# Kernel optimization log

Measured on AMD Instinct MI355X. Metric: run time of the kernel, lower is better.

## Reference

```python
import jax, jax.numpy as jnp
import numpy as np


def setup_inputs() -> dict:
    key = jax.random.key(0)
    x = jax.random.normal(key, (8192, 4096), dtype=jnp.float32)
    return {"x": x}


def reference(x) -> jnp.ndarray:
    # Sparsemax along the last axis (dim=-1), matching the torch module's math.
    n = x.shape[-1]
    x = x - jnp.max(x, axis=-1, keepdims=True)
    # sort descending
    zs = jnp.flip(jnp.sort(x, axis=-1), axis=-1)  # [B, N]
    r = jnp.arange(1, n + 1, dtype=x.dtype)       # [N]
    bound = 1.0 + r * zs
    cum_zs = jnp.cumsum(zs, axis=-1)
    is_gt = (bound > cum_zs).astype(x.dtype)
    k = jnp.max(is_gt * r, axis=-1, keepdims=True)          # support size
    taus = (jnp.sum(is_gt * zs, axis=-1, keepdims=True) - 1.0) / k
    return jnp.maximum(jnp.zeros_like(x), x - taus)
```

## Files before the change

### kernel.cpp

```cpp
#include <hip/hip_runtime.h>


#define COLS 4096
#define THREADS 256
#define NW 4
#define CAND_CAP 1024
#define MAX_ITERS 32

typedef float f32x4 __attribute__((ext_vector_type(4)));

__global__ __launch_bounds__(THREADS) void sparsemax_kernel(
    const float* __restrict__ x, float* __restrict__ out) {
  __shared__ float cand[CAND_CAP];
  __shared__ float wmax[NW];
  __shared__ float wsum[NW];
  __shared__ int wcnt[NW];
  __shared__ int cnt;

  const int tid = threadIdx.x;
  const int lane = tid & 63;
  const int wid = tid >> 6;
  const long row = blockIdx.x;

  const f32x4* __restrict__ xr =
      reinterpret_cast<const f32x4*>(x + row * COLS);
  f32x4* __restrict__ outr = reinterpret_cast<f32x4*>(out + row * COLS);

  if (tid == 0) cnt = 0;

  f32x4 v0 = xr[tid];
  f32x4 v1 = xr[tid + THREADS];
  f32x4 v2 = xr[tid + 2 * THREADS];
  f32x4 v3 = xr[tid + 3 * THREADS];

  float m = fmaxf(fmaxf(v0.x, v0.y), fmaxf(v0.z, v0.w));
  m = fmaxf(m, fmaxf(fmaxf(v1.x, v1.y), fmaxf(v1.z, v1.w)));
  m = fmaxf(m, fmaxf(fmaxf(v2.x, v2.y), fmaxf(v2.z, v2.w)));
  m = fmaxf(m, fmaxf(fmaxf(v3.x, v3.y), fmaxf(v3.z, v3.w)));
#pragma unroll
  for (int off = 32; off > 0; off >>= 1) m = fmaxf(m, __shfl_xor(m, off));
  if (lane == 0) wmax[wid] = m;
  __syncthreads();
  m = fmaxf(fmaxf(wmax[0], wmax[1]), fmaxf(wmax[2], wmax[3]));

  const float thr = m - 1.0f;

#define EMIT(val)                                   \
  if ((val) > thr) {                                \
    int p = atomicAdd(&cnt, 1);                     \
    if (p < CAND_CAP) cand[p] = (val);              \
  }
  EMIT(v0.x) EMIT(v0.y) EMIT(v0.z) EMIT(v0.w)
  EMIT(v1.x) EMIT(v1.y) EMIT(v1.z) EMIT(v1.w)
  EMIT(v2.x) EMIT(v2.y) EMIT(v2.z) EMIT(v2.w)
  EMIT(v3.x) EMIT(v3.y) EMIT(v3.z) EMIT(v3.w)
#undef EMIT
  __syncthreads();
  const int nc = cnt;

  float tau = thr;
  if (nc <= CAND_CAP) {
    for (int it = 0; it < MAX_ITERS; ++it) {
      float s = 0.0f;
      int c = 0;
      for (int k = lane; k < nc; k += 64) {
        float q = cand[k];
        if (q > tau) { s += q; c += 1; }
      }
#pragma unroll
      for (int off = 32; off > 0; off >>= 1) {
        s += __shfl_xor(s, off);
        c += __shfl_xor(c, off);
      }
      float ntau = (s - 1.0f) / (float)c;
      if (ntau == tau) break;
      tau = ntau;
    }
  } else {
    for (int it = 0; it < MAX_ITERS; ++it) {
      float s = 0.0f;
      int c = 0;
#define ACC(val)                      \
  if ((val) > tau) { s += (val); c += 1; }
      ACC(v0.x) ACC(v0.y) ACC(v0.z) ACC(v0.w)
      ACC(v1.x) ACC(v1.y) ACC(v1.z) ACC(v1.w)
      ACC(v2.x) ACC(v2.y) ACC(v2.z) ACC(v2.w)
      ACC(v3.x) ACC(v3.y) ACC(v3.z) ACC(v3.w)
#undef ACC
#pragma unroll
      for (int off = 32; off > 0; off >>= 1) {
        s += __shfl_xor(s, off);
        c += __shfl_xor(c, off);
      }
      if (lane == 0) { wsum[wid] = s; wcnt[wid] = c; }
      __syncthreads();
      s = wsum[0] + wsum[1] + wsum[2] + wsum[3];
      c = wcnt[0] + wcnt[1] + wcnt[2] + wcnt[3];
      float ntau = (s - 1.0f) / (float)c;
      __syncthreads();
      if (ntau == tau) break;
      tau = ntau;
    }
  }

  f32x4 o;
  o.x = fmaxf(v0.x - tau, 0.0f); o.y = fmaxf(v0.y - tau, 0.0f);
  o.z = fmaxf(v0.z - tau, 0.0f); o.w = fmaxf(v0.w - tau, 0.0f);
  __builtin_nontemporal_store(o, outr + tid);
  o.x = fmaxf(v1.x - tau, 0.0f); o.y = fmaxf(v1.y - tau, 0.0f);
  o.z = fmaxf(v1.z - tau, 0.0f); o.w = fmaxf(v1.w - tau, 0.0f);
  __builtin_nontemporal_store(o, outr + tid + THREADS);
  o.x = fmaxf(v2.x - tau, 0.0f); o.y = fmaxf(v2.y - tau, 0.0f);
  o.z = fmaxf(v2.z - tau, 0.0f); o.w = fmaxf(v2.w - tau, 0.0f);
  __builtin_nontemporal_store(o, outr + tid + 2 * THREADS);
  o.x = fmaxf(v3.x - tau, 0.0f); o.y = fmaxf(v3.y - tau, 0.0f);
  o.z = fmaxf(v3.z - tau, 0.0f); o.w = fmaxf(v3.w - tau, 0.0f);
  __builtin_nontemporal_store(o, outr + tid + 3 * THREADS);
}

extern "C" void kernel_launch(void* const* d_in, const int* in_sizes, int n_in,
                              void* d_out, int out_size, void* d_ws,
                              size_t ws_size, hipStream_t stream) {
  const float* x = (const float*)d_in[0];
  float* out = (float*)d_out;
  const int rows = in_sizes[0] / COLS;
  sparsemax_kernel<<<rows, THREADS, 0, stream>>>(x, out);
}
```

Measured before the change: 231.3 us.

## Split sparsemax into a tau-computation kernel and a separate apply kernel

Splits the fused kernel in two. The first kernel reads each row, finds the threshold tau (only wave 0 iterates over the candidate list) and writes it to workspace. The second kernel rereads x, applies max(x - tau, 0) across four rows per block and writes the output. The intent is to shorten the critical path of each kernel, but it adds a second full read of the input and a kernel launch.

```diff
diff --git a/kernel.cpp b/kernel.cpp
--- a/kernel.cpp
+++ b/kernel.cpp
@@ -6,25 +6,25 @@
 #define NW 4
 #define CAND_CAP 1024
 #define MAX_ITERS 32
+#define APPLY_ROWS 4
 
 typedef float f32x4 __attribute__((ext_vector_type(4)));
 
-__global__ __launch_bounds__(THREADS) void sparsemax_kernel(
-    const float* __restrict__ x, float* __restrict__ out) {
+__global__ __launch_bounds__(THREADS) void tau_kernel(
+    const float* __restrict__ x, float* __restrict__ taus, int rows) {
   __shared__ float cand[CAND_CAP];
-  __shared__ float wmax[NW];
-  __shared__ float wsum[NW];
-  __shared__ int wcnt[NW];
+  __shared__ float wred[NW];
+  __shared__ int wcnt_s[NW];
   __shared__ int cnt;
 
   const int tid = threadIdx.x;
   const int lane = tid & 63;
   const int wid = tid >> 6;
   const long row = blockIdx.x;
+  if (row >= rows) return;
 
   const f32x4* __restrict__ xr =
       reinterpret_cast<const f32x4*>(x + row * COLS);
-  f32x4* __restrict__ outr = reinterpret_cast<f32x4*>(out + row * COLS);
 
   if (tid == 0) cnt = 0;
 
@@ -39,16 +39,16 @@
   m = fmaxf(m, fmaxf(fmaxf(v3.x, v3.y), fmaxf(v3.z, v3.w)));
 #pragma unroll
   for (int off = 32; off > 0; off >>= 1) m = fmaxf(m, __shfl_xor(m, off));
-  if (lane == 0) wmax[wid] = m;
+  if (lane == 0) wred[wid] = m;
   __syncthreads();
-  m = fmaxf(fmaxf(wmax[0], wmax[1]), fmaxf(wmax[2], wmax[3]));
+  m = fmaxf(fmaxf(wred[0], wred[1]), fmaxf(wred[2], wred[3]));
 
   const float thr = m - 1.0f;
 
-#define EMIT(val)                                   \
-  if ((val) > thr) {                                \
-    int p = atomicAdd(&cnt, 1);                     \
-    if (p < CAND_CAP) cand[p] = (val);              \
+#define EMIT(val)                          \
+  if ((val) > thr) {                       \
+    int p = atomicAdd(&cnt, 1);            \
+    if (p < CAND_CAP) cand[p] = (val);     \
   }
   EMIT(v0.x) EMIT(v0.y) EMIT(v0.z) EMIT(v0.w)
   EMIT(v1.x) EMIT(v1.y) EMIT(v1.z) EMIT(v1.w)
@@ -60,28 +60,30 @@
 
   float tau = thr;
   if (nc <= CAND_CAP) {
-    for (int it = 0; it < MAX_ITERS; ++it) {
-      float s = 0.0f;
-      int c = 0;
-      for (int k = lane; k < nc; k += 64) {
-        float q = cand[k];
-        if (q > tau) { s += q; c += 1; }
+    if (wid == 0) {
+      for (int it = 0; it < MAX_ITERS; ++it) {
+        float s = 0.0f;
+        int c = 0;
+        for (int k = lane; k < nc; k += 64) {
+          float q = cand[k];
+          if (q > tau) { s += q; c += 1; }
+        }
+#pragma unroll
+        for (int off = 32; off > 0; off >>= 1) {
+          s += __shfl_xor(s, off);
+          c += __shfl_xor(c, off);
+        }
+        float ntau = (s - 1.0f) / (float)c;
+        if (ntau == tau) break;
+        tau = ntau;
       }
-#pragma unroll
-      for (int off = 32; off > 0; off >>= 1) {
-        s += __shfl_xor(s, off);
-        c += __shfl_xor(c, off);
-      }
-      float ntau = (s - 1.0f) / (float)c;
-      if (ntau == tau) break;
-      tau = ntau;
+      if (lane == 0) taus[row] = tau;
     }
   } else {
     for (int it = 0; it < MAX_ITERS; ++it) {
       float s = 0.0f;
       int c = 0;
-#define ACC(val)                      \
-  if ((val) > tau) { s += (val); c += 1; }
+#define ACC(val) if ((val) > tau) { s += (val); c += 1; }
       ACC(v0.x) ACC(v0.y) ACC(v0.z) ACC(v0.w)
       ACC(v1.x) ACC(v1.y) ACC(v1.z) ACC(v1.w)
       ACC(v2.x) ACC(v2.y) ACC(v2.z) ACC(v2.w)
@@ -92,30 +94,44 @@
         s += __shfl_xor(s, off);
         c += __shfl_xor(c, off);
       }
-      if (lane == 0) { wsum[wid] = s; wcnt[wid] = c; }
+      if (lane == 0) { wred[wid] = s; wcnt_s[wid] = c; }
       __syncthreads();
-      s = wsum[0] + wsum[1] + wsum[2] + wsum[3];
-      c = wcnt[0] + wcnt[1] + wcnt[2] + wcnt[3];
+      s = wred[0] + wred[1] + wred[2] + wred[3];
+      c = wcnt_s[0] + wcnt_s[1] + wcnt_s[2] + wcnt_s[3];
       float ntau = (s - 1.0f) / (float)c;
       __syncthreads();
       if (ntau == tau) break;
       tau = ntau;
     }
+    if (tid == 0) taus[row] = tau;
   }
+}
 
-  f32x4 o;
-  o.x = fmaxf(v0.x - tau, 0.0f); o.y = fmaxf(v0.y - tau, 0.0f);
-  o.z = fmaxf(v0.z - tau, 0.0f); o.w = fmaxf(v0.w - tau, 0.0f);
-  __builtin_nontemporal_store(o, outr + tid);
-  o.x = fmaxf(v1.x - tau, 0.0f); o.y = fmaxf(v1.y - tau, 0.0f);
-  o.z = fmaxf(v1.z - tau, 0.0f); o.w = fmaxf(v1.w - tau, 0.0f);
-  __builtin_nontemporal_store(o, outr + tid + THREADS);
-  o.x = fmaxf(v2.x - tau, 0.0f); o.y = fmaxf(v2.y - tau, 0.0f);
-  o.z = fmaxf(v2.z - tau, 0.0f); o.w = fmaxf(v2.w - tau, 0.0f);
-  __builtin_nontemporal_store(o, outr + tid + 2 * THREADS);
-  o.x = fmaxf(v3.x - tau, 0.0f); o.y = fmaxf(v3.y - tau, 0.0f);
-  o.z = fmaxf(v3.z - tau, 0.0f); o.w = fmaxf(v3.w - tau, 0.0f);
-  __builtin_nontemporal_store(o, outr + tid + 3 * THREADS);
+__global__ __launch_bounds__(THREADS) void apply_kernel(
+    const float* __restrict__ x, const float* __restrict__ taus,
+    float* __restrict__ out) {
+  const long base_row = (long)blockIdx.x * APPLY_ROWS;
+  const float t0 = taus[base_row + 0];
+  const float t1 = taus[base_row + 1];
+  const float t2 = taus[base_row + 2];
+  const float t3 = taus[base_row + 3];
+
+  const f32x4* __restrict__ xr =
+      reinterpret_cast<const f32x4*>(x + base_row * COLS);
+  f32x4* __restrict__ outr = reinterpret_cast<f32x4*>(out + base_row * COLS);
+  const int tid = threadIdx.x;
+
+#pragma unroll
+  for (int k = 0; k < 16; ++k) {
+    const float tk = (k < 4) ? t0 : (k < 8) ? t1 : (k < 12) ? t2 : t3;
+    f32x4 v = xr[tid + k * THREADS];
+    f32x4 o;
+    o.x = fmaxf(v.x - tk, 0.0f);
+    o.y = fmaxf(v.y - tk, 0.0f);
+    o.z = fmaxf(v.z - tk, 0.0f);
+    o.w = fmaxf(v.w - tk, 0.0f);
+    __builtin_nontemporal_store(o, outr + tid + k * THREADS);
+  }
 }
 
 extern "C" void kernel_launch(void* const* d_in, const int* in_sizes, int n_in,
@@ -123,6 +139,8 @@
                               size_t ws_size, hipStream_t stream) {
   const float* x = (const float*)d_in[0];
   float* out = (float*)d_out;
+  float* taus = (float*)d_ws;
   const int rows = in_sizes[0] / COLS;
-  sparsemax_kernel<<<rows, THREADS, 0, stream>>>(x, out);
+  tau_kernel<<<rows, THREADS, 0, stream>>>(x, taus, rows);
+  apply_kernel<<<rows / APPLY_ROWS, THREADS, 0, stream>>>(x, taus, out);
 }
```

Result: slower. 239.4 us (+3.5%).
